# Optimization experiments

Hardware: AMD Instinct MI355X
Metric: run time of the kernel (lower is better)

Reference implementation:

```python
import jax, jax.numpy as jnp
import numpy as np

B, H, W, C = 16, 48, 48, 256
D_INNER = 2 * C          # ssm_ratio = 2.0
D_STATE = 1
DT_RANK = C // 16        # mamba convention: dt_rank = d_model // 16
HID = 4 * C              # mlp_ratio = 4.0
N = H * W


def _grid_neighbors(h, w):
    idx = np.arange(h * w).reshape(h, w)
    pad_r = -np.ones((1, w), np.int64)
    pad_c = -np.ones((h, 1), np.int64)
    up = np.concatenate([pad_r, idx[:-1]], 0)
    down = np.concatenate([idx[1:], pad_r], 0)
    left = np.concatenate([pad_c, idx[:, :-1]], 1)
    right = np.concatenate([idx[:, 1:], pad_c], 1)
    nb = np.stack([up, down, left, right], -1).reshape(h * w, 4)
    valid = nb >= 0
    return jnp.asarray(np.where(valid, nb, 0), np.int32), jnp.asarray(valid)

_NBR, _VALID = _grid_neighbors(H, W)


def _mst(x):
    """Input-adaptive MST (Prim) on the 4-connected pixel grid.
    Edge weight = exp(1 - cosine_similarity) between adjacent pixel features.
    Returns (order, par): Prim insertion order (a valid BFS-like topological order:
    every node's parent appears earlier) and parent node id per node."""
    b = x.shape[0]
    f = x.reshape(b, N, C)
    f = f / (jnp.linalg.norm(f, axis=-1, keepdims=True) + 1e-8)
    cos = jnp.einsum('bnc,bnkc->bnk', f, f[:, _NBR])          # (B,N,4)
    wgt = jnp.where(_VALID, jnp.exp(1.0 - cos), jnp.inf)

    def prim(wb):
        key = jnp.full((N,), jnp.inf, wb.dtype).at[0].set(0.0)
        par = jnp.zeros((N,), jnp.int32)
        intree = jnp.zeros((N,), bool)

        def step(carry, _):
            key, par, intree = carry
            u = jnp.argmin(jnp.where(intree, jnp.inf, key)).astype(jnp.int32)
            intree = intree.at[u].set(True)
            nb, wv = _NBR[u], wb[u]
            better = (~intree[nb]) & (wv < key[nb])
            key = key.at[nb].set(jnp.where(better, wv, key[nb]))
            par = par.at[nb].set(jnp.where(better, u, par[nb]))
            return (key, par, intree), u

        (_, par, _), order = jax.lax.scan(step, (key, par, intree), None, length=N)
        return order, par

    return jax.vmap(prim)(wgt)


def _ln(x, g, b):
    m = jnp.mean(x, -1, keepdims=True)
    v = jnp.var(x, -1, keepdims=True)
    return (x - m) * jax.lax.rsqrt(v + 1e-5) * g + b


def _tree_ssm(xn, order, par, W_in, b_in, W_xp, W_dt, b_dt, A_log, Dp, W_out, b_out):
    """Mamba-style selective scan generalized to a tree: the hidden state of node v
    recurses from its MST parent instead of the previous sequence position."""
    b = xn.shape[0]
    xf = xn.reshape(b, N, C)
    xz = xf @ W_in + b_in                               # (B,N,2*D_INNER)
    xi, z = xz[..., :D_INNER], xz[..., D_INNER:]
    xi = jax.nn.silu(xi)
    dbc = xi @ W_xp                                     # (B,N,DT_RANK+2)
    dtr = dbc[..., :DT_RANK]
    Bv = dbc[..., DT_RANK:DT_RANK + 1]                  # d_state = 1
    Cv = dbc[..., DT_RANK + 1:DT_RANK + 2]
    dt = jax.nn.softplus(dtr @ W_dt + b_dt)             # (B,N,D_INNER)
    A = -jnp.exp(A_log)                                 # (D_INNER,)
    decay = jnp.exp(dt * A)
    Bx = dt * Bv * xi

    def tree_scan(ob, pb, db, xb):
        def step(hbuf, v):
            hv = db[v] * hbuf[pb[v]] + xb[v]            # h[v] = decay*h[parent] + B*x
            return hbuf.at[v].set(hv), None
        hbuf, _ = jax.lax.scan(step, jnp.zeros((N, D_INNER), db.dtype), ob)
        return hbuf

    h = jax.vmap(tree_scan)(order, par, decay, Bx)      # (B,N,D_INNER)
    y = Cv * h + Dp * xi
    return ((y * jax.nn.silu(z)) @ W_out + b_out).reshape(xn.shape)


def setup_inputs():
    key = jax.random.key(0)
    ks = jax.random.split(key, 8)
    g = lambda k, shp, s=0.02: jax.random.normal(k, shp, jnp.float32) * s
    return {
        "x": jax.random.normal(ks[0], (B, H, W, C), jnp.float32),
        "norm1_w": jnp.ones((C,), jnp.float32), "norm1_b": jnp.zeros((C,), jnp.float32),
        "norm2_w": jnp.ones((C,), jnp.float32), "norm2_b": jnp.zeros((C,), jnp.float32),
        "W_in": g(ks[1], (C, 2 * D_INNER)), "b_in": jnp.zeros((2 * D_INNER,), jnp.float32),
        "W_xp": g(ks[2], (D_INNER, DT_RANK + 2 * D_STATE)),
        "W_dt": g(ks[3], (DT_RANK, D_INNER), 0.1), "b_dt": jnp.full((D_INNER,), -2.0, jnp.float32),
        "A_log": jnp.zeros((D_INNER,), jnp.float32), "Dp": jnp.ones((D_INNER,), jnp.float32),
        "W_out": g(ks[4], (D_INNER, C)), "b_out": jnp.zeros((C,), jnp.float32),
        "fc1_w": g(ks[5], (C, HID)), "fc1_b": jnp.zeros((HID,), jnp.float32),
        "fc2_w": g(ks[6], (HID, C)), "fc2_b": jnp.zeros((C,), jnp.float32),
    }


def reference(x, norm1_w, norm1_b, norm2_w, norm2_b, W_in, b_in, W_xp, W_dt, b_dt,
              A_log, Dp, W_out, b_out, fc1_w, fc1_b, fc2_w, fc2_b):
    order, par = _mst(jax.lax.stop_gradient(x))         # torch.no_grad() MST
    x = x + _tree_ssm(_ln(x, norm1_w, norm1_b), order, par,
                      W_in, b_in, W_xp, W_dt, b_dt, A_log, Dp, W_out, b_out)
    h = jax.nn.gelu(_ln(x, norm2_w, norm2_b) @ fc1_w + fc1_b, approximate=False)
    return x + h @ fc2_w + fc2_b
```

## Files before the change

kernel.cpp:

```cpp
#include <hip/hip_runtime.h>
#include <math.h>

#define NN 2304
#define BB 16
#define CC 256
#define DI 512
#define MM (BB*NN)

typedef __attribute__((ext_vector_type(8))) short bf16x8;
typedef __attribute__((ext_vector_type(4))) float f32x4;

__device__ inline unsigned short f2b(float f){
  unsigned u = __float_as_uint(f);
  u = u + 0x7FFFu + ((u>>16)&1u);
  return (unsigned short)(u>>16);
}
__device__ inline float b2f(unsigned short s){ return __uint_as_float(((unsigned)s)<<16); }
__device__ __forceinline__ int dstep(int d){ return (d==0)?-48:(d==1)?48:(d==2)?-1:1; }

__global__ __launch_bounds__(256) void k_wconv(const float* __restrict__ in, unsigned short* __restrict__ out, int R, int Ccols){
  int idx = blockIdx.x*256 + threadIdx.x;
  if (idx >= R*Ccols) return;
  int r = idx / Ccols, c = idx - r*Ccols;
  out[(size_t)c*R + r] = f2b(in[idx]);
}
__global__ __launch_bounds__(256) void k_t32(const float* __restrict__ in, float* __restrict__ out, int R, int Ccols){
  int idx = blockIdx.x*256 + threadIdx.x;
  if (idx >= R*Ccols) return;
  int r = idx / Ccols, c = idx - r*Ccols;
  out[(size_t)c*R + r] = in[idx];
}

__global__ __launch_bounds__(256) void k_norm(const float* __restrict__ x, float* __restrict__ innorm){
  int row = blockIdx.x*4 + (threadIdx.x>>6); int lane = threadIdx.x&63;
  float4 v = *(const float4*)(x + (size_t)row*CC + lane*4);
  float s = v.x*v.x + v.y*v.y + v.z*v.z + v.w*v.w;
  #pragma unroll
  for (int o=32;o;o>>=1) s += __shfl_xor(s,o);
  if (lane==0) innorm[row] = 1.0f/(sqrtf(s)+1e-8f);
}

__global__ __launch_bounds__(256) void k_edge(const float* __restrict__ x, const float* __restrict__ innorm, float* __restrict__ wgt){
  int g = blockIdx.x*4 + (threadIdx.x>>6); int lane = threadIdx.x&63;
  int b = g/NN, n = g - b*NN;
  int r = n/48, c = n - (n/48)*48;
  const float* xb = x + ((size_t)b*NN)*CC;
  float4 vu = *(const float4*)(xb + (size_t)n*CC + lane*4);
  int nb0=(r>0)?n-48:-1, nb1=(r<47)?n+48:-1, nb2=(c>0)?n-1:-1, nb3=(c<47)?n+1:-1;
  float d0=0,d1=0,d2=0,d3=0;
  if (nb0>=0){ float4 t=*(const float4*)(xb+(size_t)nb0*CC+lane*4); d0=vu.x*t.x+vu.y*t.y+vu.z*t.z+vu.w*t.w; }
  if (nb1>=0){ float4 t=*(const float4*)(xb+(size_t)nb1*CC+lane*4); d1=vu.x*t.x+vu.y*t.y+vu.z*t.z+vu.w*t.w; }
  if (nb2>=0){ float4 t=*(const float4*)(xb+(size_t)nb2*CC+lane*4); d2=vu.x*t.x+vu.y*t.y+vu.z*t.z+vu.w*t.w; }
  if (nb3>=0){ float4 t=*(const float4*)(xb+(size_t)nb3*CC+lane*4); d3=vu.x*t.x+vu.y*t.y+vu.z*t.z+vu.w*t.w; }
  #pragma unroll
  for (int o=32;o;o>>=1){ d0+=__shfl_xor(d0,o); d1+=__shfl_xor(d1,o); d2+=__shfl_xor(d2,o); d3+=__shfl_xor(d3,o); }
  if (lane==0){
    float inu = innorm[g];
    float inf_ = __uint_as_float(0x7F800000u);
    float4 w;
    w.x = (nb0>=0)? expf(1.0f - d0*(inu*innorm[g-n+nb0])) : inf_;
    w.y = (nb1>=0)? expf(1.0f - d1*(inu*innorm[g-n+nb1])) : inf_;
    w.z = (nb2>=0)? expf(1.0f - d2*(inu*innorm[g-n+nb2])) : inf_;
    w.w = (nb3>=0)? expf(1.0f - d3*(inu*innorm[g-n+nb3])) : inf_;
    *(float4*)(wgt + (size_t)g*4) = w;
  }
}

#define INFB 0x7F800000u
#define NILA 0x3FFFu
__device__ void mst_body(unsigned char* smem, const float* __restrict__ wgt, int b,
    unsigned short* __restrict__ parpos_g, int* __restrict__ lvlorder,
    int* __restrict__ lvlstart, int* __restrict__ nlvl)
{
  unsigned* tmask = (unsigned*)smem;
  unsigned* pk    = (unsigned*)(smem + 9216);
  unsigned* comp   = pk;
  unsigned* bestw  = pk + 2304;
  unsigned* bestid = pk + 4608;
  unsigned short* par   = (unsigned short*)(smem + 46080);
  unsigned short* dpos  = (unsigned short*)(smem + 50688);
  int* hist = (int*)(smem + 55296);
  int* ctr  = (int*)(smem + 64512);
  const int tid = threadIdx.x;
  const float* wb = wgt + (size_t)b*NN*4;

  #pragma unroll
  for (int k=0;k<9;k++){ int v=tid+k*256; comp[v]=v; tmask[v]=0u; }
  __syncthreads();

  for (int round=0; round<14; round++){
    #pragma unroll
    for (int k=0;k<9;k++){ int v=tid+k*256; bestw[v]=INFB; bestid[v]=0xFFFFFFFFu; }
    __syncthreads();
    unsigned candw[9], candi[9];
    #pragma unroll
    for (int k=0;k<9;k++){
      int v=tid+k*256;
      unsigned cv=comp[v];
      int r=v/48, c=v-(v/48)*48;
      float4 w4 = *(const float4*)(wb + (size_t)v*4);
      unsigned cw=INFB, ci=0xFFFFFFFFu;
      if (r>0  && comp[v-48]!=cv){ unsigned wv=__float_as_uint(w4.x); if (wv<cw){cw=wv;ci=(unsigned)(v*4+0);} }
      if (r<47 && comp[v+48]!=cv){ unsigned wv=__float_as_uint(w4.y); if (wv<cw){cw=wv;ci=(unsigned)(v*4+1);} }
      if (c>0  && comp[v-1] !=cv){ unsigned wv=__float_as_uint(w4.z); if (wv<cw){cw=wv;ci=(unsigned)(v*4+2);} }
      if (c<47 && comp[v+1] !=cv){ unsigned wv=__float_as_uint(w4.w); if (wv<cw){cw=wv;ci=(unsigned)(v*4+3);} }
      candw[k]=cw; candi[k]=ci;
      if (cw!=INFB) atomicMin(&bestw[cv], cw);
    }
    __syncthreads();
    #pragma unroll
    for (int k=0;k<9;k++){
      if (candw[k]!=INFB){
        int v=tid+k*256; unsigned cv=comp[v];
        if (bestw[cv]==candw[k]) atomicMin(&bestid[cv], candi[k]);
      }
    }
    __syncthreads();
    unsigned hookS[9];
    #pragma unroll
    for (int k=0;k<9;k++){
      int v=tid+k*256; hookS[k]=0xFFFFFFFFu;
      if (comp[v]!=(unsigned)v) continue;
      unsigned id=bestid[v];
      if (id==0xFFFFFFFFu) continue;
      int u=(int)(id>>2), d=(int)(id&3);
      int o = u + dstep(d);
      unsigned s = comp[o];
      unsigned sid = bestid[s];
      bool mutual=false;
      if (sid!=0xFFFFFFFFu){
        int su=(int)(sid>>2), sd=(int)(sid&3);
        int so = su + dstep(sd);
        mutual = (comp[so]==(unsigned)v);
      }
      if (!mutual || (unsigned)v>s) hookS[k]=s;
    }
    __syncthreads();
    #pragma unroll
    for (int k=0;k<9;k++){
      if (hookS[k]==0xFFFFFFFFu) continue;
      int v=tid+k*256;
      unsigned id=bestid[v];
      int u=(int)(id>>2), d=(int)(id&3);
      int o = u + dstep(d);
      comp[v]=hookS[k];
      atomicOr(&tmask[u], 1u<<d);
      atomicOr(&tmask[o], 1u<<(d^1));
    }
    __syncthreads();
    for (int it=0; it<16; it++){
      if (tid==0) ctr[1]=0;
      __syncthreads();
      int ch=0;
      #pragma unroll
      for (int k=0;k<9;k++){
        int v=tid+k*256;
        unsigned c1=comp[v], c2=comp[c1];
        if (c1!=c2){ comp[v]=c2; ch=1; }
      }
      if (ch) atomicAdd(&ctr[1],1);
      __syncthreads();
      if (ctr[1]==0) break;
    }
    if (tid==0) ctr[2]=0;
    __syncthreads();
    int rc=0;
    #pragma unroll
    for (int k=0;k<9;k++){ int v=tid+k*256; if (comp[v]==(unsigned)v) rc++; }
    if (rc) atomicAdd(&ctr[2], rc);
    __syncthreads();
    if (ctr[2]<=1) break;
  }
  __syncthreads();

  int a0;
  { unsigned m0 = tmask[0]; a0 = __ffs((int)(m0&0xFu))-1; }

  for (int pass=0; pass<2; pass++){
    for (int k=0;k<36;k++){
      int a = k*256+tid;
      int v = a>>2, d = a&3;
      unsigned mv = tmask[v];
      unsigned sc = NILA;
      unsigned vl = pass ? 8192u : 0u;
      if ((mv>>d)&1u){
        int w = v + dstep(d);
        unsigned mw = tmask[w];
        int rd = d^1;
        int nd = -1;
        #pragma unroll
        for (int kk=1;kk<=4;kk++){ int c2=(rd+kk)&3; if (nd<0 && ((mw>>c2)&1u)) nd=c2; }
        sc = (unsigned)(w*4+nd);
        if (sc==(unsigned)a0) sc=NILA;
        vl = pass ? (8192u + (((mv>>(4+d))&1u)? 1u : (unsigned)-1)) : 1u;
      }
      pk[a] = (sc<<14) | (vl & 0x3FFFu);
    }
    __syncthreads();
    for (int it=0; it<13; it++){
      unsigned stg[36];
      #pragma unroll
      for (int k=0;k<36;k++){
        int a=k*256+tid;
        unsigned mine=pk[a];
        unsigned s=mine>>14;
        if (s==NILA) stg[k]=mine;
        else {
          unsigned oth=pk[s];
          unsigned nv=(mine&0x3FFFu)+(oth&0x3FFFu);
          if (pass) nv -= 8192u;
          stg[k]=((oth>>14)<<14)|(nv&0x3FFFu);
        }
      }
      __syncthreads();
      #pragma unroll
      for (int k=0;k<36;k++) pk[k*256+tid]=stg[k];
      __syncthreads();
    }
    if (pass==0){
      for (int k=0;k<36;k++){
        int a=k*256+tid;
        int v=a>>2, d=a&3;
        if ((tmask[v]>>d)&1u){
          int w=v+dstep(d);
          int ra=w*4+(d^1);
          if ((pk[a]&0x3FFFu) > (pk[ra]&0x3FFFu)){
            atomicOr(&tmask[v], 16u<<d);
            par[w]=(unsigned short)v;
          }
        }
      }
      __syncthreads();
    }
  }
  if (tid==0){ par[0]=0; dpos[0]=0; ctr[3]=0; }
  __syncthreads();
  for (int k=0;k<36;k++){
    int a=k*256+tid;
    int v=a>>2, d=a&3;
    unsigned mv=tmask[v];
    if (((mv>>d)&1u) && ((mv>>(4+d))&1u)){
      int w=v+dstep(d);
      int S=(int)(pk[a]&0x3FFFu)-8192;
      int dep=1-S;
      dpos[w]=(unsigned short)dep;
      atomicMax(&ctr[3],dep);
    }
  }
  __syncthreads();
  int nlv_=ctr[3]+1;
  for (int i=tid;i<nlv_;i+=256) hist[i]=0;
  __syncthreads();
  for (int i=tid;i<NN;i+=256) atomicAdd(&hist[dpos[i]],1);
  __syncthreads();
  if (tid==0){
    int run=0;
    for (int l=0;l<nlv_;l++){ int c2=hist[l]; hist[l]=run; lvlstart[b*(NN+2)+l]=run; run+=c2; }
    lvlstart[b*(NN+2)+nlv_]=run;
    nlvl[b]=nlv_;
  }
  __syncthreads();
  for (int i=tid;i<NN;i+=256){
    int pos=atomicAdd(&hist[dpos[i]],1);
    lvlorder[b*NN+pos]=i;
    dpos[i]=(unsigned short)pos;
  }
  __syncthreads();
  for (int i=tid;i<NN;i+=256)
    parpos_g[b*NN + dpos[i]] = dpos[par[i]];
}

template<int EPI>
__device__ void gemm_body(unsigned short* lA, unsigned short* lB, int bm, int bn,
    const unsigned short* __restrict__ A, const unsigned short* __restrict__ BT,
    const float* __restrict__ bias, int Ndim, int K,
    const float* __restrict__ addin, float* __restrict__ fout,
    unsigned short* __restrict__ bout0, unsigned short* __restrict__ bout1,
    const int* __restrict__ lvl)
{
  int tid=threadIdx.x, wid=tid>>6, lane=tid&63;
  const unsigned short* Ab = A + (size_t)bm*128*K;
  const unsigned short* Bb = BT + (size_t)bn*128*K;
  int wr=wid>>1, wc=wid&1;
  f32x4 acc[4][4];
  #pragma unroll
  for (int m2=0;m2<4;m2++)
    #pragma unroll
    for (int n2=0;n2<4;n2++)
      #pragma unroll
      for (int j=0;j<4;j++) acc[m2][n2][j]=0.f;
  int r0 = tid>>2, c0 = (tid&3)*8;
  for (int k0=0;k0<K;k0+=32){
    int4 va0 = *(const int4*)(Ab + (size_t)r0*K + k0 + c0);
    int4 va1 = *(const int4*)(Ab + (size_t)(r0+64)*K + k0 + c0);
    int4 vb0 = *(const int4*)(Bb + (size_t)r0*K + k0 + c0);
    int4 vb1 = *(const int4*)(Bb + (size_t)(r0+64)*K + k0 + c0);
    __syncthreads();
    *(int4*)(lA + r0*32 + c0) = va0;
    *(int4*)(lA + (r0+64)*32 + c0) = va1;
    *(int4*)(lB + r0*32 + c0) = vb0;
    *(int4*)(lB + (r0+64)*32 + c0) = vb1;
    __syncthreads();
    int ra = (wr<<6) + (lane&15);
    int rb = (wc<<6) + (lane&15);
    int cb = (lane>>4)<<3;
    bf16x8 af[4], bfr[4];
    #pragma unroll
    for (int m2=0;m2<4;m2++) af[m2] = *(const bf16x8*)(lA + (ra+m2*16)*32 + cb);
    #pragma unroll
    for (int n2=0;n2<4;n2++) bfr[n2] = *(const bf16x8*)(lB + (rb+n2*16)*32 + cb);
    #pragma unroll
    for (int m2=0;m2<4;m2++)
      #pragma unroll
      for (int n2=0;n2<4;n2++)
        acc[m2][n2] = __builtin_amdgcn_mfma_f32_16x16x32_bf16(af[m2], bfr[n2], acc[m2][n2], 0,0,0);
  }
  int rr = (lane>>4)<<2, cc = lane&15;
  #pragma unroll
  for (int m2=0;m2<4;m2++){
    #pragma unroll
    for (int n2=0;n2<4;n2++){
      int col = (bn<<7) + (wc<<6) + (n2<<4) + cc;
      float bs = bias[col];
      #pragma unroll
      for (int j=0;j<4;j++){
        int row = (bm<<7) + (wr<<6) + (m2<<4) + rr + j;
        float v = acc[m2][n2][j] + bs;
        if (EPI==0){
          float sv = v * (1.0f/(1.0f+expf(-v)));
          if (col < DI) bout0[(size_t)row*DI + col] = f2b(sv);
          else          bout1[(size_t)row*DI + col - DI] = f2b(sv);
        } else if (EPI==1){
          size_t oi=(size_t)row*Ndim+col;
          fout[oi] = addin[oi] + v;
        } else if (EPI==2){
          size_t oi=(size_t)row*Ndim+col;
          bout0[oi] = f2b(0.5f*v*(1.0f+erff(v*0.70710678118f)));
        } else if (EPI==3){
          int grow = (row/NN)*NN + lvl[row];
          fout[(size_t)row*Ndim+col] = addin[(size_t)grow*Ndim+col] + v;
        } else {
          int grow = (row/NN)*NN + lvl[row];
          fout[(size_t)grow*Ndim+col] = addin[(size_t)row*Ndim+col] + v;
        }
      }
    }
  }
}

template<int EPI>
__global__ __launch_bounds__(256) void k_gemm(
    const unsigned short* __restrict__ A, const unsigned short* __restrict__ BT,
    const float* __restrict__ bias, int Ndim, int K,
    const float* __restrict__ addin, float* __restrict__ fout,
    unsigned short* __restrict__ bout0, unsigned short* __restrict__ bout1,
    const int* __restrict__ lvl)
{
  __shared__ __align__(16) unsigned short lAB[128*32*2];
  int ntn = Ndim>>7;
  int bm = blockIdx.x/ntn, bn = blockIdx.x - bm*ntn;
  gemm_body<EPI>(lAB, lAB+128*32, bm, bn, A, BT, bias, Ndim, K, addin, fout, bout0, bout1, lvl);
}

__global__ __launch_bounds__(256) void k_fused(
    const unsigned short* __restrict__ xn, const unsigned short* __restrict__ WinT,
    const float* __restrict__ b_in,
    unsigned short* __restrict__ xi_b, unsigned short* __restrict__ sz_b,
    const float* __restrict__ wgt, unsigned short* __restrict__ parpos_g,
    int* __restrict__ lvlorder, int* __restrict__ lvlstart, int* __restrict__ nlvl)
{
  __shared__ __align__(16) unsigned char smem[64528];
  if (blockIdx.x < BB){
    mst_body(smem, wgt, blockIdx.x, parpos_g, lvlorder, lvlstart, nlvl);
  } else {
    int bid = blockIdx.x - BB;
    int bm = bid>>3, bn = bid&7;
    gemm_body<0>((unsigned short*)smem, (unsigned short*)smem + 128*32, bm, bn,
                 xn, WinT, b_in, 1024, 256, nullptr, nullptr, xi_b, sz_b, nullptr);
  }
}

__global__ __launch_bounds__(256) void k_ln(const float* __restrict__ xin, const float* __restrict__ g,
    const float* __restrict__ bta, unsigned short* __restrict__ outb)
{
  int row = blockIdx.x*4 + (threadIdx.x>>6); int lane=threadIdx.x&63;
  float4 v = *(const float4*)(xin + (size_t)row*CC + lane*4);
  float s = v.x+v.y+v.z+v.w;
  #pragma unroll
  for (int o=32;o;o>>=1) s += __shfl_xor(s,o);
  float m = s*(1.0f/256.0f);
  float dx=v.x-m, dy=v.y-m, dz=v.z-m, dw=v.w-m;
  float ss=dx*dx+dy*dy+dz*dz+dw*dw;
  #pragma unroll
  for (int o=32;o;o>>=1) ss += __shfl_xor(ss,o);
  float rs = rsqrtf(ss*(1.0f/256.0f)+1e-5f);
  int cb=lane*4;
  unsigned o0 = (unsigned)f2b(dx*rs*g[cb+0]+bta[cb+0]) | ((unsigned)f2b(dy*rs*g[cb+1]+bta[cb+1])<<16);
  unsigned o1 = (unsigned)f2b(dz*rs*g[cb+2]+bta[cb+2]) | ((unsigned)f2b(dw*rs*g[cb+3]+bta[cb+3])<<16);
  *(uint2*)(outb + (size_t)row*CC + cb) = make_uint2(o0,o1);
}

__global__ __launch_bounds__(256) void k_dbc(const unsigned short* __restrict__ xi_b,
    const float* __restrict__ WxpT, float* __restrict__ dbc)
{
  int row = blockIdx.x*4 + (threadIdx.x>>6); int lane=threadIdx.x&63;
  int4 raw = *(const int4*)(xi_b + (size_t)row*DI + lane*8);
  float xf[8];
  xf[0]=b2f((unsigned short)((unsigned)raw.x&0xFFFFu)); xf[1]=b2f((unsigned short)((unsigned)raw.x>>16));
  xf[2]=b2f((unsigned short)((unsigned)raw.y&0xFFFFu)); xf[3]=b2f((unsigned short)((unsigned)raw.y>>16));
  xf[4]=b2f((unsigned short)((unsigned)raw.z&0xFFFFu)); xf[5]=b2f((unsigned short)((unsigned)raw.z>>16));
  xf[6]=b2f((unsigned short)((unsigned)raw.w&0xFFFFu)); xf[7]=b2f((unsigned short)((unsigned)raw.w>>16));
  for (int jc=0;jc<18;jc++){
    const float* wr_ = WxpT + (size_t)jc*DI + lane*8;
    float s=0.f;
    #pragma unroll
    for (int t=0;t<8;t++) s += xf[t]*wr_[t];
    #pragma unroll
    for (int o=32;o;o>>=1) s += __shfl_xor(s,o);
    if (lane==0) dbc[(size_t)row*18+jc]=s;
  }
}

__global__ __launch_bounds__(512) void k_dbx(const float* __restrict__ dbc, const unsigned short* __restrict__ xi_b,
  const float* __restrict__ W_dt, const float* __restrict__ b_dt, const float* __restrict__ A_log,
  const int* __restrict__ lvlorder,
  unsigned short* __restrict__ dec_cm, unsigned short* __restrict__ bx_cm)
{
  __shared__ int smap[32];
  __shared__ float sd[32][18];
  int c = threadIdx.x;
  int b = blockIdx.x/72, pg = blockIdx.x - b*72;
  int p0 = pg*32;
  if (c<32) smap[c] = b*NN + lvlorder[b*NN + p0 + c];
  __syncthreads();
  for (int i=c;i<32*18;i+=512){ int rr=i/18, q=i-rr*18; sd[rr][q]=dbc[(size_t)smap[rr]*18+q]; }
  __syncthreads();
  float wdt[16];
  #pragma unroll
  for (int r2=0;r2<16;r2++) wdt[r2]=W_dt[r2*DI+c];
  float bd=b_dt[c];
  float nA=-expf(A_log[c]);
  unsigned decp[16], bxp[16];
  #pragma unroll
  for (int rr=0;rr<32;rr++){
    float a=bd;
    #pragma unroll
    for (int r2=0;r2<16;r2++) a += sd[rr][r2]*wdt[r2];
    float dt = (a>20.f)? a : log1pf(expf(a));
    float dec = expf(dt*nA);
    float bx = dt*sd[rr][16]*b2f(xi_b[(size_t)smap[rr]*DI + c]);
    if (rr&1){ decp[rr>>1] |= ((unsigned)f2b(dec))<<16; bxp[rr>>1] |= ((unsigned)f2b(bx))<<16; }
    else     { decp[rr>>1]  =  (unsigned)f2b(dec);      bxp[rr>>1]  =  (unsigned)f2b(bx); }
  }
  size_t chb = ((size_t)b*DI + c)*NN + p0;
  uint4* dp = (uint4*)(dec_cm + chb);
  uint4* bp = (uint4*)(bx_cm + chb);
  #pragma unroll
  for (int q=0;q<4;q++){
    uint4 dv, bv;
    dv.x=decp[q*4+0]; dv.y=decp[q*4+1]; dv.z=decp[q*4+2]; dv.w=decp[q*4+3];
    bv.x=bxp[q*4+0];  bv.y=bxp[q*4+1];  bv.z=bxp[q*4+2];  bv.w=bxp[q*4+3];
    dp[q]=dv; bp[q]=bv;
  }
}

#define SCH 4
__global__ __launch_bounds__(256) void k_scan(const unsigned short* __restrict__ dec_cm,
    unsigned short* __restrict__ bx_cm,
    const unsigned short* __restrict__ parpos_g,
    const int* __restrict__ lvlstart, const int* __restrict__ nlvl)
{
  __shared__ unsigned short sdec[SCH*NN];
  __shared__ unsigned short sbx[SCH*NN];
  __shared__ unsigned short spp[NN];
  int b = blockIdx.x>>7, t = blockIdx.x&127;
  int c0 = t*SCH;
  int tid = threadIdx.x;
  const size_t gch = ((size_t)b*DI + c0)*NN;
  #pragma unroll
  for (int cc=0;cc<SCH;cc++){
    const uint2* gd = (const uint2*)(dec_cm + gch + (size_t)cc*NN);
    const uint2* gb = (const uint2*)(bx_cm + gch + (size_t)cc*NN);
    uint2* ld = (uint2*)(sdec + cc*NN);
    uint2* lb = (uint2*)(sbx + cc*NN);
    for (int i=tid;i<NN/4;i+=256){ ld[i]=gd[i]; lb[i]=gb[i]; }
  }
  for (int i=tid;i<NN;i+=256) spp[i]=parpos_g[b*NN+i];
  int nlv = nlvl[b];
  __syncthreads();
  for (int lvl=1; lvl<nlv; lvl++){
    int s=lvlstart[b*(NN+2)+lvl], e=lvlstart[b*(NN+2)+lvl+1];
    int tot=(e-s)*SCH;
    for (int idx=tid; idx<tot; idx+=256){
      int p = s + (idx>>2);
      int cc = idx&3;
      int pp = spp[p];
      float hv = b2f(sdec[cc*NN+p])*b2f(sbx[cc*NN+pp]) + b2f(sbx[cc*NN+p]);
      sbx[cc*NN+p] = f2b(hv);
    }
    __syncthreads();
  }
  #pragma unroll
  for (int cc=0;cc<SCH;cc++){
    uint2* gb = (uint2*)(bx_cm + gch + (size_t)cc*NN);
    const uint2* lb = (const uint2*)(sbx + cc*NN);
    for (int i=tid;i<NN/4;i+=256) gb[i]=lb[i];
  }
}

__global__ __launch_bounds__(512) void k_u(const unsigned short* __restrict__ h_cm,
    const unsigned short* __restrict__ xi_b, const unsigned short* __restrict__ sz_b,
    const float* __restrict__ dbc, const float* __restrict__ Dp,
    const int* __restrict__ lvlorder, unsigned short* __restrict__ u_perm)
{
  __shared__ int smap[32];
  __shared__ unsigned short hT[32*512];
  int c = threadIdx.x;
  int b = blockIdx.x/72, pg = blockIdx.x - b*72;
  int p0 = pg*32;
  if (c<32) smap[c] = b*NN + lvlorder[b*NN + p0 + c];
  {
    const uint4* gh = (const uint4*)(h_cm + ((size_t)b*DI + c)*NN + p0);
    #pragma unroll
    for (int q=0;q<4;q++){
      uint4 w = gh[q];
      unsigned ws[4] = {w.x,w.y,w.z,w.w};
      #pragma unroll
      for (int e=0;e<4;e++){
        hT[(q*8+e*2+0)*512 + c] = (unsigned short)(ws[e]&0xFFFFu);
        hT[(q*8+e*2+1)*512 + c] = (unsigned short)(ws[e]>>16);
      }
    }
  }
  float dpc = Dp[c];
  __syncthreads();
  #pragma unroll 4
  for (int rr=0;rr<32;rr++){
    int grow = smap[rr];
    float Cv = dbc[(size_t)grow*18+17];
    float xiv = b2f(xi_b[(size_t)grow*DI + c]);
    float szv = b2f(sz_b[(size_t)grow*DI + c]);
    float hv = b2f(hT[rr*512 + c]);
    float u = (Cv*hv + dpc*xiv)*szv;
    u_perm[((size_t)(b*NN + p0 + rr))*DI + c] = f2b(u);
  }
}

extern "C" void kernel_launch(void* const* d_in, const int* in_sizes, int n_in,
                              void* d_out, int out_size, void* d_ws, size_t ws_size,
                              hipStream_t stream) {
  (void)in_sizes; (void)n_in; (void)out_size; (void)ws_size;
  const float* x      = (const float*)d_in[0];
  const float* n1w    = (const float*)d_in[1];
  const float* n1b    = (const float*)d_in[2];
  const float* n2w    = (const float*)d_in[3];
  const float* n2b    = (const float*)d_in[4];
  const float* W_in   = (const float*)d_in[5];
  const float* b_in   = (const float*)d_in[6];
  const float* W_xp   = (const float*)d_in[7];
  const float* W_dt   = (const float*)d_in[8];
  const float* b_dt   = (const float*)d_in[9];
  const float* A_log  = (const float*)d_in[10];
  const float* Dp     = (const float*)d_in[11];
  const float* W_out  = (const float*)d_in[12];
  const float* b_out  = (const float*)d_in[13];
  const float* fc1_w  = (const float*)d_in[14];
  const float* fc1_b  = (const float*)d_in[15];
  const float* fc2_w  = (const float*)d_in[16];
  const float* fc2_b  = (const float*)d_in[17];

  char* base=(char*)d_ws; size_t off=0;
  auto alc=[&](size_t nb)->char*{ char* p=base+off; off=(off+nb+255)&~(size_t)255; return p; };
  float* wgt            = (float*)alc((size_t)MM*4*4);
  float* innorm         = (float*)alc((size_t)MM*4);
  unsigned short* parpos= (unsigned short*)alc((size_t)MM*2);
  int* lvlorder         = (int*)alc((size_t)MM*4);
  int* lvlstart         = (int*)alc((size_t)BB*(NN+2)*4);
  int* nlvl             = (int*)alc((size_t)BB*4);
  unsigned short* xi_b  = (unsigned short*)alc((size_t)MM*DI*2);
  unsigned short* sz_b  = (unsigned short*)alc((size_t)MM*DI*2);
  float* dbc            = (float*)alc((size_t)MM*18*4);
  unsigned short* dec_cm= (unsigned short*)alc((size_t)MM*DI*2);
  unsigned short* bx_cm = (unsigned short*)alc((size_t)MM*DI*2);
  unsigned short* WinT  = (unsigned short*)alc((size_t)CC*1024*2);
  unsigned short* WoutT = (unsigned short*)alc((size_t)DI*CC*2);
  unsigned short* fc1T  = (unsigned short*)alc((size_t)CC*1024*2);
  unsigned short* fc2T  = (unsigned short*)alc((size_t)1024*CC*2);
  float* WxpT           = (float*)alc((size_t)DI*18*4);
  unsigned short* xn      = (unsigned short*)dec_cm;
  unsigned short* h_cm    = bx_cm;
  unsigned short* u_perm  = dec_cm;
  float* x2_perm          = (float*)bx_cm;
  unsigned short* x2n_perm= dec_cm;
  unsigned short* g1_perm = xi_b;

  k_wconv<<<dim3((256*1024+255)/256),dim3(256),0,stream>>>(W_in, WinT, 256,1024);
  k_wconv<<<dim3((512*256 +255)/256),dim3(256),0,stream>>>(W_out, WoutT, 512,256);
  k_wconv<<<dim3((256*1024+255)/256),dim3(256),0,stream>>>(fc1_w, fc1T, 256,1024);
  k_wconv<<<dim3((1024*256+255)/256),dim3(256),0,stream>>>(fc2_w, fc2T, 1024,256);
  k_t32  <<<dim3((512*18  +255)/256),dim3(256),0,stream>>>(W_xp, WxpT, 512,18);

  k_norm<<<dim3(MM/4),dim3(256),0,stream>>>(x, innorm);
  k_edge<<<dim3(MM/4),dim3(256),0,stream>>>(x, innorm, wgt);
  k_ln<<<dim3(MM/4),dim3(256),0,stream>>>(x, n1w, n1b, xn);

  k_fused<<<dim3(BB + 288*8),dim3(256),0,stream>>>(xn, WinT, b_in, xi_b, sz_b,
                                                   wgt, parpos, lvlorder, lvlstart, nlvl);

  k_dbc<<<dim3(MM/4),dim3(256),0,stream>>>(xi_b, WxpT, dbc);
  k_dbx<<<dim3(MM/32),dim3(512),0,stream>>>(dbc, xi_b, W_dt, b_dt, A_log, lvlorder, dec_cm, bx_cm);
  k_scan<<<dim3(BB*128),dim3(256),0,stream>>>(dec_cm, bx_cm, parpos, lvlstart, nlvl);
  k_u<<<dim3(MM/32),dim3(512),0,stream>>>(h_cm, xi_b, sz_b, dbc, Dp, lvlorder, u_perm);

  k_gemm<3><<<dim3(288*2),dim3(256),0,stream>>>(u_perm, WoutT, b_out, 256, 512,
                                                x, x2_perm, nullptr, nullptr, lvlorder);
  k_ln<<<dim3(MM/4),dim3(256),0,stream>>>(x2_perm, n2w, n2b, x2n_perm);
  k_gemm<2><<<dim3(288*8),dim3(256),0,stream>>>(x2n_perm, fc1T, fc1_b, 1024, 256,
                                                nullptr, nullptr, g1_perm, nullptr, nullptr);
  k_gemm<4><<<dim3(288*2),dim3(256),0,stream>>>(g1_perm, fc2T, fc2_b, 256, 1024,
                                                x2_perm, (float*)d_out, nullptr, nullptr, lvlorder);
}
```

Baseline: 729.7 us.

## Run Boruvka MST in a single wavefront and load GEMM tiles directly into LDS

The Boruvka MST rounds now run on one 64-lane wavefront using wave barriers instead of block-wide __syncthreads. A packed 64-bit weight|id key with a single atomicMin replaces the two-pass min-weight/min-id reduction. The aim is to cut the many block barriers and atomic passes on the serial MST critical path, at the cost of each lane handling 36 vertices instead of 9. The GEMM tile loads switch to global_load_lds (direct global-to-LDS 16-byte loads), removing the register round trip. The wave-contiguous LDS destination layout this uses has to line up with the fragment reads.

```diff
diff --git a/kernel.cpp b/kernel.cpp
--- a/kernel.cpp
+++ b/kernel.cpp
@@ -17,6 +17,12 @@
 }
 __device__ inline float b2f(unsigned short s){ return __uint_as_float(((unsigned)s)<<16); }
 __device__ __forceinline__ int dstep(int d){ return (d==0)?-48:(d==1)?48:(d==2)?-1:1; }
+
+__device__ __forceinline__ void gld16(const void* g, void* l){
+  __builtin_amdgcn_global_load_lds((const __attribute__((address_space(1))) void*)g,
+                                   (__attribute__((address_space(3))) void*)l, 16, 0, 0);
+}
+#define WF() { __builtin_amdgcn_wave_barrier(); __builtin_amdgcn_sched_barrier(0); }
 
 __global__ __launch_bounds__(256) void k_wconv(const float* __restrict__ in, unsigned short* __restrict__ out, int R, int Ccols){
   int idx = blockIdx.x*256 + threadIdx.x;
@@ -74,9 +80,9 @@
 {
   unsigned* tmask = (unsigned*)smem;
   unsigned* pk    = (unsigned*)(smem + 9216);
-  unsigned* comp   = pk;
-  unsigned* bestw  = pk + 2304;
-  unsigned* bestid = pk + 4608;
+  unsigned* comp  = pk;
+  unsigned long long* bestk = (unsigned long long*)(smem + 18432);
+  unsigned* hookd = (unsigned*)(smem + 36864);
   unsigned short* par   = (unsigned short*)(smem + 46080);
   unsigned short* dpos  = (unsigned short*)(smem + 50688);
   int* hist = (int*)(smem + 55296);
@@ -88,88 +94,80 @@
   for (int k=0;k<9;k++){ int v=tid+k*256; comp[v]=v; tmask[v]=0u; }
   __syncthreads();
 
-  for (int round=0; round<14; round++){
-    #pragma unroll
-    for (int k=0;k<9;k++){ int v=tid+k*256; bestw[v]=INFB; bestid[v]=0xFFFFFFFFu; }
-    __syncthreads();
-    unsigned candw[9], candi[9];
-    #pragma unroll
-    for (int k=0;k<9;k++){
-      int v=tid+k*256;
-      unsigned cv=comp[v];
-      int r=v/48, c=v-(v/48)*48;
-      float4 w4 = *(const float4*)(wb + (size_t)v*4);
-      unsigned cw=INFB, ci=0xFFFFFFFFu;
-      if (r>0  && comp[v-48]!=cv){ unsigned wv=__float_as_uint(w4.x); if (wv<cw){cw=wv;ci=(unsigned)(v*4+0);} }
-      if (r<47 && comp[v+48]!=cv){ unsigned wv=__float_as_uint(w4.y); if (wv<cw){cw=wv;ci=(unsigned)(v*4+1);} }
-      if (c>0  && comp[v-1] !=cv){ unsigned wv=__float_as_uint(w4.z); if (wv<cw){cw=wv;ci=(unsigned)(v*4+2);} }
-      if (c<47 && comp[v+1] !=cv){ unsigned wv=__float_as_uint(w4.w); if (wv<cw){cw=wv;ci=(unsigned)(v*4+3);} }
-      candw[k]=cw; candi[k]=ci;
-      if (cw!=INFB) atomicMin(&bestw[cv], cw);
-    }
-    __syncthreads();
-    #pragma unroll
-    for (int k=0;k<9;k++){
-      if (candw[k]!=INFB){
-        int v=tid+k*256; unsigned cv=comp[v];
-        if (bestw[cv]==candw[k]) atomicMin(&bestid[cv], candi[k]);
-      }
-    }
-    __syncthreads();
-    unsigned hookS[9];
-    #pragma unroll
-    for (int k=0;k<9;k++){
-      int v=tid+k*256; hookS[k]=0xFFFFFFFFu;
-      if (comp[v]!=(unsigned)v) continue;
-      unsigned id=bestid[v];
-      if (id==0xFFFFFFFFu) continue;
-      int u=(int)(id>>2), d=(int)(id&3);
-      int o = u + dstep(d);
-      unsigned s = comp[o];
-      unsigned sid = bestid[s];
-      bool mutual=false;
-      if (sid!=0xFFFFFFFFu){
-        int su=(int)(sid>>2), sd=(int)(sid&3);
-        int so = su + dstep(sd);
-        mutual = (comp[so]==(unsigned)v);
-      }
-      if (!mutual || (unsigned)v>s) hookS[k]=s;
-    }
-    __syncthreads();
-    #pragma unroll
-    for (int k=0;k<9;k++){
-      if (hookS[k]==0xFFFFFFFFu) continue;
-      int v=tid+k*256;
-      unsigned id=bestid[v];
-      int u=(int)(id>>2), d=(int)(id&3);
-      int o = u + dstep(d);
-      comp[v]=hookS[k];
-      atomicOr(&tmask[u], 1u<<d);
-      atomicOr(&tmask[o], 1u<<(d^1));
-    }
-    __syncthreads();
-    for (int it=0; it<16; it++){
-      if (tid==0) ctr[1]=0;
-      __syncthreads();
-      int ch=0;
-      #pragma unroll
-      for (int k=0;k<9;k++){
-        int v=tid+k*256;
-        unsigned c1=comp[v], c2=comp[c1];
-        if (c1!=c2){ comp[v]=c2; ch=1; }
-      }
-      if (ch) atomicAdd(&ctr[1],1);
-      __syncthreads();
-      if (ctr[1]==0) break;
-    }
-    if (tid==0) ctr[2]=0;
-    __syncthreads();
-    int rc=0;
-    #pragma unroll
-    for (int k=0;k<9;k++){ int v=tid+k*256; if (comp[v]==(unsigned)v) rc++; }
-    if (rc) atomicAdd(&ctr[2], rc);
-    __syncthreads();
-    if (ctr[2]<=1) break;
+  if (tid < 64){
+    volatile unsigned* vcomp = comp;
+    volatile unsigned long long* vbk = bestk;
+    volatile unsigned* vhk = hookd;
+    const int lane = tid;
+    for (int round=0; round<14; round++){
+      for (int k=0;k<36;k++) bestk[k*64+lane] = ~0ull;
+      WF();
+      #pragma unroll 4
+      for (int k=0;k<36;k++){
+        int v=k*64+lane;
+        unsigned cv=vcomp[v];
+        int r=v/48, c=v-(v/48)*48;
+        float4 w4 = *(const float4*)(wb + (size_t)v*4);
+        unsigned long long best=~0ull;
+        if (r>0 ){ unsigned o=vcomp[v-48]; if(o!=cv){ unsigned long long kk=((unsigned long long)__float_as_uint(w4.x)<<32)|(unsigned)(v*4+0); if(kk<best)best=kk; } }
+        if (r<47){ unsigned o=vcomp[v+48]; if(o!=cv){ unsigned long long kk=((unsigned long long)__float_as_uint(w4.y)<<32)|(unsigned)(v*4+1); if(kk<best)best=kk; } }
+        if (c>0 ){ unsigned o=vcomp[v-1];  if(o!=cv){ unsigned long long kk=((unsigned long long)__float_as_uint(w4.z)<<32)|(unsigned)(v*4+2); if(kk<best)best=kk; } }
+        if (c<47){ unsigned o=vcomp[v+1];  if(o!=cv){ unsigned long long kk=((unsigned long long)__float_as_uint(w4.w)<<32)|(unsigned)(v*4+3); if(kk<best)best=kk; } }
+        if (best!=~0ull) atomicMin((unsigned long long*)&bestk[cv], best);
+      }
+      WF();
+      for (int k=0;k<36;k++){
+        int v=k*64+lane;
+        unsigned hd=0xFFFFFFFFu;
+        if (vcomp[v]==(unsigned)v){
+          unsigned long long key=vbk[v];
+          if (key!=~0ull){
+            unsigned id=(unsigned)key;
+            int u=(int)(id>>2), d=(int)(id&3);
+            int o = u + dstep(d);
+            unsigned s=vcomp[o];
+            unsigned long long sk=vbk[s];
+            bool mutual=false;
+            if (sk!=~0ull){
+              unsigned sid=(unsigned)sk;
+              int su=(int)(sid>>2), sd=(int)(sid&3);
+              int so = su + dstep(sd);
+              mutual = (vcomp[so]==(unsigned)v);
+            }
+            if (!mutual || (unsigned)v>s) hd=s;
+          }
+        }
+        vhk[v]=hd;
+      }
+      WF();
+      for (int k=0;k<36;k++){
+        int v=k*64+lane;
+        unsigned s=vhk[v];
+        if (s!=0xFFFFFFFFu){
+          unsigned id=(unsigned)vbk[v];
+          int u=(int)(id>>2), d=(int)(id&3);
+          int o = u + dstep(d);
+          vcomp[v]=s;
+          atomicOr(&tmask[u], 1u<<d);
+          atomicOr(&tmask[o], 1u<<(d^1));
+        }
+      }
+      WF();
+      for (int it=0; it<20; it++){
+        int ch=0;
+        for (int k=0;k<36;k++){
+          int v=k*64+lane;
+          unsigned c1=vcomp[v], c2=vcomp[c1];
+          if (c1!=c2){ vcomp[v]=c2; ch=1; }
+        }
+        WF();
+        if (!__any(ch)) break;
+      }
+      unsigned rr=vcomp[0];
+      int bad=0;
+      for (int k=0;k<36;k++){ if (vcomp[k*64+lane]!=rr) bad=1; }
+      if (!__any(bad)) break;
+    }
   }
   __syncthreads();
 
@@ -271,7 +269,7 @@
 }
 
 template<int EPI>
-__device__ void gemm_body(unsigned short* lA, unsigned short* lB, int bm, int bn,
+__device__ void gemm_body(unsigned short* lAB, int bm, int bn,
     const unsigned short* __restrict__ A, const unsigned short* __restrict__ BT,
     const float* __restrict__ bias, int Ndim, int K,
     const float* __restrict__ addin, float* __restrict__ fout,
@@ -290,16 +288,15 @@
       #pragma unroll
       for (int j=0;j<4;j++) acc[m2][n2][j]=0.f;
   int r0 = tid>>2, c0 = (tid&3)*8;
+  unsigned short* lA = lAB;
+  unsigned short* lB = lAB + 4096;
+  unsigned short* dstA = lAB + wid*512;
   for (int k0=0;k0<K;k0+=32){
-    int4 va0 = *(const int4*)(Ab + (size_t)r0*K + k0 + c0);
-    int4 va1 = *(const int4*)(Ab + (size_t)(r0+64)*K + k0 + c0);
-    int4 vb0 = *(const int4*)(Bb + (size_t)r0*K + k0 + c0);
-    int4 vb1 = *(const int4*)(Bb + (size_t)(r0+64)*K + k0 + c0);
     __syncthreads();
-    *(int4*)(lA + r0*32 + c0) = va0;
-    *(int4*)(lA + (r0+64)*32 + c0) = va1;
-    *(int4*)(lB + r0*32 + c0) = vb0;
-    *(int4*)(lB + (r0+64)*32 + c0) = vb1;
+    gld16(Ab + (size_t)r0*K + k0 + c0,        dstA);
+    gld16(Ab + (size_t)(r0+64)*K + k0 + c0,   dstA + 2048);
+    gld16(Bb + (size_t)r0*K + k0 + c0,        dstA + 4096);
+    gld16(Bb + (size_t)(r0+64)*K + k0 + c0,   dstA + 6144);
     __syncthreads();
     int ra = (wr<<6) + (lane&15);
     int rb = (wc<<6) + (lane&15);
@@ -356,10 +353,10 @@
     unsigned short* __restrict__ bout0, unsigned short* __restrict__ bout1,
     const int* __restrict__ lvl)
 {
-  __shared__ __align__(16) unsigned short lAB[128*32*2];
+  __shared__ __align__(16) unsigned short lAB[8192];
   int ntn = Ndim>>7;
   int bm = blockIdx.x/ntn, bn = blockIdx.x - bm*ntn;
-  gemm_body<EPI>(lAB, lAB+128*32, bm, bn, A, BT, bias, Ndim, K, addin, fout, bout0, bout1, lvl);
+  gemm_body<EPI>(lAB, bm, bn, A, BT, bias, Ndim, K, addin, fout, bout0, bout1, lvl);
 }
 
 __global__ __launch_bounds__(256) void k_fused(
@@ -375,7 +372,7 @@
   } else {
     int bid = blockIdx.x - BB;
     int bm = bid>>3, bn = bid&7;
-    gemm_body<0>((unsigned short*)smem, (unsigned short*)smem + 128*32, bm, bn,
+    gemm_body<0>((unsigned short*)smem, bm, bn,
                  xn, WinT, b_in, 1024, 256, nullptr, nullptr, xi_b, sz_b, nullptr);
   }
 }
```

New measurement: 945.1 us. 29.5% more time.
